# Kernel tuning notes

Measured on AMD Instinct MI355X. Metric: run time of the kernel, lower is better.

Reference implementation:

```python
import math
import jax, jax.numpy as jnp
import numpy as np

NUM_HEADS = 16
BASE = 10000.0


def _rope_sin_cos(seq_len, head_dim):
    # theta_j = pos / base^(2j/dim), j in [0, dim//2)
    j = jnp.arange(head_dim // 2, dtype=jnp.float32)
    inv_freq = jnp.power(jnp.float32(BASE), -2.0 * j / head_dim)  # [d/2]
    pos = jnp.arange(seq_len, dtype=jnp.float32)
    ang = pos[:, None] * inv_freq[None, :]          # [S, d/2]
    sin, cos = jnp.sin(ang), jnp.cos(ang)
    # interleave-repeat each entry twice: [S, d]
    sin2 = jnp.stack([sin, sin], axis=-1).reshape(seq_len, head_dim)
    cos2 = jnp.stack([cos, cos], axis=-1).reshape(seq_len, head_dim)
    return sin2, cos2


def _apply_rope(x, sin2, cos2):
    # x: [B, H, S, d]; rotate-half interleaved: (-x1, x0, -x3, x2, ...)
    x_even, x_odd = x[..., 0::2], x[..., 1::2]
    rot = jnp.stack([-x_odd, x_even], axis=-1).reshape(x.shape)
    return x * cos2 + rot * sin2


def setup_inputs() -> dict:
    key = jax.random.key(0)
    ks = jax.random.split(key, 9)
    B, S, H = 2, 2048, 2048
    sc = 1.0 / math.sqrt(H)
    return {
        "hidden_state": jax.random.normal(ks[0], (B, S, H), jnp.float32),
        "Wq": jax.random.normal(ks[1], (H, H), jnp.float32) * sc,
        "bq": jax.random.normal(ks[2], (H,), jnp.float32) * 0.01,
        "Wk": jax.random.normal(ks[3], (H, H), jnp.float32) * sc,
        "bk": jax.random.normal(ks[4], (H,), jnp.float32) * 0.01,
        "Wv": jax.random.normal(ks[5], (H, H), jnp.float32) * sc,
        "bv": jax.random.normal(ks[6], (H,), jnp.float32) * 0.01,
        "Wo": jax.random.normal(ks[7], (H, H), jnp.float32) * sc,
        "bo": jax.random.normal(ks[8], (H,), jnp.float32) * 0.01,
    }


def reference(hidden_state, Wq, bq, Wk, bk, Wv, bv, Wo, bo):
    B, S, H = hidden_state.shape
    nh = NUM_HEADS
    hd = H // nh

    def proj(W, b):
        y = jnp.einsum('bsh,hd->bsd', hidden_state, W) + b
        return y.reshape(B, S, nh, hd).transpose(0, 2, 1, 3)  # [B,nh,S,hd]

    q = proj(Wq, bq)
    k = proj(Wk, bk)
    v = proj(Wv, bv)

    sin2, cos2 = _rope_sin_cos(S, hd)  # [S, hd]
    q = _apply_rope(q, sin2, cos2)
    k = _apply_rope(k, sin2, cos2)

    scale = 1.0 / math.sqrt(hd)
    attn = jnp.einsum('bhqd,bhkd->bhqk', q, k) * scale  # [B,nh,S,S]
    attn = jax.nn.softmax(attn, axis=-1)
    out = jnp.einsum('bhqk,bhkd->bhqd', attn, v)
    out = out.transpose(0, 2, 1, 3).reshape(B, S, H)
    return jnp.einsum('bsh,hd->bsd', out, Wo) + bo
```

## Files before the change

### kernel.cpp

```cpp
#include <hip/hip_runtime.h>
#include <math.h>


typedef __bf16 bf16;
typedef __attribute__((ext_vector_type(8))) __bf16 bf16x8;
typedef __attribute__((ext_vector_type(4))) __bf16 bf16x4;
typedef __attribute__((ext_vector_type(4))) float f32x4;

#define S_LEN 2048
#define NHEAD 16
#define HD 128

__device__ __forceinline__ f32x4 mfma16(bf16x8 a, bf16x8 b, f32x4 c) {
    return __builtin_amdgcn_mfma_f32_16x16x32_bf16(a, b, c, 0, 0, 0);
}

__global__ __launch_bounds__(256) void cvt_f32_bf16(const float* __restrict__ x,
                                                    bf16* __restrict__ y, int n) {
    int i = (blockIdx.x * 256 + threadIdx.x) * 4;
    if (i + 3 < n) {
        const float4 v = *(const float4*)(x + i);
        bf16x4 o;
        o[0] = (bf16)v.x; o[1] = (bf16)v.y; o[2] = (bf16)v.z; o[3] = (bf16)v.w;
        *(bf16x4*)(y + i) = o;
    }
}

__global__ __launch_bounds__(128) void rope_tables(float* __restrict__ st,
                                                   float* __restrict__ ct) {
    const int s = blockIdx.x, d = threadIdx.x;
    const float invf = exp2f(-0.20762050593046013f * (float)(d >> 1));
    float sn, cs;
    sincosf((float)s * invf, &sn, &cs);
    st[(s << 7) | d] = sn;
    ct[(s << 7) | d] = cs;
}

__global__ __launch_bounds__(256) void transpose_cvt(const float* __restrict__ W,
                                                     bf16* __restrict__ Wt,
                                                     int Kd, int Nd) {
    __shared__ float tile[32][33];
    const int tx = threadIdx.x & 31, ty = threadIdx.x >> 5;
    const int bn = blockIdx.x * 32, bk = blockIdx.y * 32;
#pragma unroll
    for (int r = 0; r < 32; r += 8)
        tile[ty + r][tx] = W[(size_t)(bk + ty + r) * Nd + bn + tx];
    __syncthreads();
#pragma unroll
    for (int r = 0; r < 32; r += 8)
        Wt[(size_t)(bn + ty + r) * Kd + bk + tx] = (bf16)tile[tx][ty + r];
}

__global__ __launch_bounds__(256, 3)
void gemm_qkv(const bf16* __restrict__ A, const bf16* __restrict__ Bt,
              const float* __restrict__ bq, const float* __restrict__ bk,
              const float* __restrict__ bv, bf16* __restrict__ Qo,
              bf16* __restrict__ Ko, bf16* __restrict__ Vo,
              const float* __restrict__ stab, const float* __restrict__ ctab) {
    const int K = 2048;
    __shared__ __align__(16) bf16 smem[17408];
    bf16* As = smem;
    bf16* Bs = smem + 8192;
    const int t = threadIdx.x;
    const int w = t >> 6, l = t & 63;
    const int lr = l & 15, lq = l >> 4;
    const int m0 = blockIdx.y * 128, n0 = blockIdx.x * 128;
    const int wm = (w >> 1) * 64, wn = (w & 1) * 64;
    const int seg = n0 >> 11;
    const float* bias = (seg == 0) ? bq : (seg == 1) ? bk : bv;
    bf16* outB = (seg == 0) ? Qo : (seg == 1) ? Ko : Vo;

    f32x4 acc[4][4];
    const f32x4 fz = {0.f, 0.f, 0.f, 0.f};
#pragma unroll
    for (int i = 0; i < 4; ++i)
#pragma unroll
        for (int j = 0; j < 4; ++j) acc[i][j] = fz;

    bf16x8 rA[4], rB[4];
#pragma unroll
    for (int c = 0; c < 4; ++c) {
        const int chunk = c * 256 + t;
        const int row = chunk >> 3, cc = chunk & 7;
        rA[c] = *(const bf16x8*)&A[(size_t)(m0 + row) * K + cc * 8];
        rB[c] = *(const bf16x8*)&Bt[(size_t)(n0 + row) * K + cc * 8];
    }

    for (int k0 = 0; k0 < K; k0 += 64) {
#pragma unroll
        for (int c = 0; c < 4; ++c) {
            const int chunk = c * 256 + t;
            const int row = chunk >> 3, cc = chunk & 7;
            const int d = (row * 8 + (cc ^ (row & 7))) * 8;
            *(bf16x8*)&As[d] = rA[c];
            *(bf16x8*)&Bs[d] = rB[c];
        }
        __syncthreads();
        if (k0 + 64 < K) {
#pragma unroll
            for (int c = 0; c < 4; ++c) {
                const int chunk = c * 256 + t;
                const int row = chunk >> 3, cc = chunk & 7;
                rA[c] = *(const bf16x8*)&A[(size_t)(m0 + row) * K + k0 + 64 + cc * 8];
                rB[c] = *(const bf16x8*)&Bt[(size_t)(n0 + row) * K + k0 + 64 + cc * 8];
            }
        }
#pragma unroll
        for (int s = 0; s < 2; ++s) {
            bf16x8 af[4], bfr[4];
#pragma unroll
            for (int i = 0; i < 4; ++i) {
                const int row = wm + i * 16 + lr;
                af[i] = *(const bf16x8*)&As[(row * 8 + ((s * 4 + lq) ^ (row & 7))) * 8];
            }
#pragma unroll
            for (int j = 0; j < 4; ++j) {
                const int row = wn + j * 16 + lr;
                bfr[j] = *(const bf16x8*)&Bs[(row * 8 + ((s * 4 + lq) ^ (row & 7))) * 8];
            }
#pragma unroll
            for (int i = 0; i < 4; ++i)
#pragma unroll
                for (int j = 0; j < 4; ++j)
                    acc[i][j] = mfma16(af[i], bfr[j], acc[i][j]);
        }
        __syncthreads();
    }

    if (seg == 2) {
#pragma unroll
        for (int i = 0; i < 4; ++i) {
            const int rl0 = wm + i * 16 + lq * 4;
#pragma unroll
            for (int j = 0; j < 4; ++j) {
                const int cl = wn + j * 16 + lr;
                const float bv_ = bias[(n0 & 2047) + cl];
#pragma unroll
                for (int r = 0; r < 4; ++r)
                    smem[cl * 136 + rl0 + r] = (bf16)(acc[i][j][r] + bv_);
            }
        }
        __syncthreads();
        const int b = m0 >> 11;
#pragma unroll
        for (int p = 0; p < 8; ++p) {
            const int idx = p * 256 + t;
            const int col = idx >> 4, ch = idx & 15;
            const bf16x8 v = *(const bf16x8*)&smem[col * 136 + ch * 8];
            const int cg2 = (n0 & 2047) + col;
            const int h = cg2 >> 7, d = cg2 & 127;
            *(bf16x8*)&outB[((size_t)((b << 4) | h) * HD + d) * S_LEN +
                            (m0 & 2047) + ch * 8] = v;
        }
    } else {
#pragma unroll
        for (int i = 0; i < 4; ++i) {
            const int rg0 = m0 + wm + i * 16 + lq * 4;
#pragma unroll
            for (int j = 0; j < 4; ++j) {
                const int cg2 = (n0 & 2047) + wn + j * 16 + lr;
                const float bv_ = bias[cg2];
                const int h = cg2 >> 7, d = cg2 & 127;
#pragma unroll
                for (int r = 0; r < 4; ++r) {
                    const int rg = rg0 + r;
                    const int b = rg >> 11, s = rg & 2047;
                    float v = acc[i][j][r] + bv_;
                    float p = __shfl_xor(v, 1);
                    const float sn = stab[(s << 7) | d];
                    const float cs = ctab[(s << 7) | d];
                    float o = (d & 1) ? (v * cs + p * sn) : (v * cs - p * sn);
                    if (seg == 0) o *= 0.08838834764831843f;
                    outB[((size_t)((b << 4) + h) * S_LEN + s) * HD + d] = (bf16)o;
                }
            }
        }
    }
}

__global__ __launch_bounds__(256, 3)
void gemm_out(const bf16* __restrict__ A, const bf16* __restrict__ Bt,
              const float* __restrict__ bias, float* __restrict__ outF,
              int M, int N, int K) {
    __shared__ __align__(16) bf16 As[128 * 64];
    __shared__ __align__(16) bf16 Bs[128 * 64];
    const int t = threadIdx.x;
    const int w = t >> 6, l = t & 63;
    const int lr = l & 15, lq = l >> 4;
    const int m0 = blockIdx.y * 128, n0 = blockIdx.x * 128;
    const int wm = (w >> 1) * 64, wn = (w & 1) * 64;

    f32x4 acc[4][4];
    const f32x4 fz = {0.f, 0.f, 0.f, 0.f};
#pragma unroll
    for (int i = 0; i < 4; ++i)
#pragma unroll
        for (int j = 0; j < 4; ++j) acc[i][j] = fz;

    bf16x8 rA[4], rB[4];
#pragma unroll
    for (int c = 0; c < 4; ++c) {
        const int chunk = c * 256 + t;
        const int row = chunk >> 3, cc = chunk & 7;
        rA[c] = *(const bf16x8*)&A[(size_t)(m0 + row) * K + cc * 8];
        rB[c] = *(const bf16x8*)&Bt[(size_t)(n0 + row) * K + cc * 8];
    }

    for (int k0 = 0; k0 < K; k0 += 64) {
#pragma unroll
        for (int c = 0; c < 4; ++c) {
            const int chunk = c * 256 + t;
            const int row = chunk >> 3, cc = chunk & 7;
            const int d = (row * 8 + (cc ^ (row & 7))) * 8;
            *(bf16x8*)&As[d] = rA[c];
            *(bf16x8*)&Bs[d] = rB[c];
        }
        __syncthreads();
        if (k0 + 64 < K) {
#pragma unroll
            for (int c = 0; c < 4; ++c) {
                const int chunk = c * 256 + t;
                const int row = chunk >> 3, cc = chunk & 7;
                rA[c] = *(const bf16x8*)&A[(size_t)(m0 + row) * K + k0 + 64 + cc * 8];
                rB[c] = *(const bf16x8*)&Bt[(size_t)(n0 + row) * K + k0 + 64 + cc * 8];
            }
        }
#pragma unroll
        for (int s = 0; s < 2; ++s) {
            bf16x8 af[4], bfr[4];
#pragma unroll
            for (int i = 0; i < 4; ++i) {
                const int row = wm + i * 16 + lr;
                af[i] = *(const bf16x8*)&As[(row * 8 + ((s * 4 + lq) ^ (row & 7))) * 8];
            }
#pragma unroll
            for (int j = 0; j < 4; ++j) {
                const int row = wn + j * 16 + lr;
                bfr[j] = *(const bf16x8*)&Bs[(row * 8 + ((s * 4 + lq) ^ (row & 7))) * 8];
            }
#pragma unroll
            for (int i = 0; i < 4; ++i)
#pragma unroll
                for (int j = 0; j < 4; ++j)
                    acc[i][j] = mfma16(af[i], bfr[j], acc[i][j]);
        }
        __syncthreads();
    }
#pragma unroll
    for (int i = 0; i < 4; ++i) {
        const int rg0 = m0 + wm + i * 16 + lq * 4;
#pragma unroll
        for (int j = 0; j < 4; ++j) {
            const int cg = n0 + wn + j * 16 + lr;
            const float bv = bias[cg];
#pragma unroll
            for (int r = 0; r < 4; ++r)
                outF[(size_t)(rg0 + r) * N + cg] = acc[i][j][r] + bv;
        }
    }
}

__global__ __launch_bounds__(256, 2)
void attn_fwd(const bf16* __restrict__ Q, const bf16* __restrict__ K,
              const bf16* __restrict__ Vt, bf16* __restrict__ AO) {
    __shared__ __align__(16) bf16 Ks[64 * 128];
    __shared__ __align__(16) bf16 Vs[128 * 64];
    const int t = threadIdx.x;
    const int w = t >> 6, l = t & 63;
    const int lr = l & 15, lq = l >> 4;
    const int blk = blockIdx.x;
    const int qt = (blk >> 3) & 15;
    const int bh = ((blk & 7) << 2) | (blk >> 7);
    const int b = bh >> 4, h = bh & 15;

    const bf16* Qp = Q + (size_t)bh * S_LEN * HD;
    const bf16* Kp = K + (size_t)bh * S_LEN * HD;
    const bf16* Vp = Vt + (size_t)bh * HD * S_LEN;

    bf16x8 qf[2][4];
#pragma unroll
    for (int i = 0; i < 2; ++i)
#pragma unroll
        for (int s = 0; s < 4; ++s)
            qf[i][s] = *(const bf16x8*)&Qp[(size_t)(qt * 128 + w * 32 + i * 16 + lr) * HD +
                                           s * 32 + lq * 8];

    f32x4 O[2][8];
    const f32x4 fz = {0.f, 0.f, 0.f, 0.f};
#pragma unroll
    for (int i = 0; i < 2; ++i)
#pragma unroll
        for (int jd = 0; jd < 8; ++jd) O[i][jd] = fz;
    float lst[2][4] = {{0.f, 0.f, 0.f, 0.f}, {0.f, 0.f, 0.f, 0.f}};

    bf16x8 rK[4], rV[4];
#pragma unroll
    for (int c = 0; c < 4; ++c) {
        const int chunk = c * 256 + t;
        const int kr = chunk >> 4, kc = chunk & 15;
        const int vr = chunk >> 3, vc = chunk & 7;
        rK[c] = *(const bf16x8*)&Kp[(size_t)kr * HD + kc * 8];
        rV[c] = *(const bf16x8*)&Vp[(size_t)vr * S_LEN + vc * 8];
    }

    for (int kt = 0; kt < 32; ++kt) {
#pragma unroll
        for (int c = 0; c < 4; ++c) {
            const int chunk = c * 256 + t;
            const int kr = chunk >> 4, kc = chunk & 15;
            const int vr = chunk >> 3, vc = chunk & 7;
            *(bf16x8*)&Ks[(kr * 16 + (kc ^ (kr & 15))) * 8] = rK[c];
            *(bf16x8*)&Vs[(vr * 8 + (vc ^ (vr & 7))) * 8] = rV[c];
        }
        __syncthreads();

        if (kt < 31) {
#pragma unroll
            for (int c = 0; c < 4; ++c) {
                const int chunk = c * 256 + t;
                const int kr = chunk >> 4, kc = chunk & 15;
                const int vr = chunk >> 3, vc = chunk & 7;
                rK[c] = *(const bf16x8*)&Kp[(size_t)((kt + 1) * 64 + kr) * HD + kc * 8];
                rV[c] = *(const bf16x8*)&Vp[(size_t)vr * S_LEN + (kt + 1) * 64 + vc * 8];
            }
        }

        f32x4 Sc[2][4];
#pragma unroll
        for (int i = 0; i < 2; ++i)
#pragma unroll
            for (int j = 0; j < 4; ++j) Sc[i][j] = fz;
#pragma unroll
        for (int s = 0; s < 4; ++s) {
            bf16x8 kf[4];
#pragma unroll
            for (int j = 0; j < 4; ++j) {
                const int krow = j * 16 + lr;
                kf[j] = *(const bf16x8*)&Ks[(krow * 16 + ((s * 4 + lq) ^ (krow & 15))) * 8];
            }
#pragma unroll
            for (int i = 0; i < 2; ++i)
#pragma unroll
                for (int j = 0; j < 4; ++j)
                    Sc[i][j] = mfma16(qf[i][s], kf[j], Sc[i][j]);
        }
        __syncthreads();

        bf16* Ps = Ks;
#pragma unroll
        for (int i = 0; i < 2; ++i)
#pragma unroll
            for (int j = 0; j < 4; ++j)
#pragma unroll
                for (int r = 0; r < 4; ++r) {
                    const float p = __expf(Sc[i][j][r]);
                    lst[i][r] += p;
                    const int prow = w * 32 + i * 16 + lq * 4 + r;
                    const int pch = (j * 2 + (lr >> 3)) ^ (prow & 7);
                    Ps[(prow * 8 + pch) * 8 + (lr & 7)] = (bf16)p;
                }

#pragma unroll
        for (int s = 0; s < 2; ++s) {
            bf16x8 pf[2], vf[8];
#pragma unroll
            for (int i = 0; i < 2; ++i) {
                const int prow = w * 32 + i * 16 + lr;
                pf[i] = *(const bf16x8*)&Ps[(prow * 8 + ((s * 4 + lq) ^ (prow & 7))) * 8];
            }
#pragma unroll
            for (int jd = 0; jd < 8; ++jd) {
                const int vrow = jd * 16 + lr;
                vf[jd] = *(const bf16x8*)&Vs[(vrow * 8 + ((s * 4 + lq) ^ (vrow & 7))) * 8];
            }
#pragma unroll
            for (int i = 0; i < 2; ++i)
#pragma unroll
                for (int jd = 0; jd < 8; ++jd)
                    O[i][jd] = mfma16(pf[i], vf[jd], O[i][jd]);
        }
        __syncthreads();
    }

#pragma unroll
    for (int mask = 1; mask < 16; mask <<= 1)
#pragma unroll
        for (int i = 0; i < 2; ++i)
#pragma unroll
            for (int r = 0; r < 4; ++r) lst[i][r] += __shfl_xor(lst[i][r], mask);

#pragma unroll
    for (int i = 0; i < 2; ++i)
#pragma unroll
        for (int jd = 0; jd < 8; ++jd)
#pragma unroll
            for (int r = 0; r < 4; ++r) {
                const int srow = qt * 128 + w * 32 + i * 16 + lq * 4 + r;
                const float v = O[i][jd][r] / lst[i][r];
                AO[(size_t)(b * S_LEN + srow) * 2048 + h * HD + jd * 16 + lr] = (bf16)v;
            }
}

extern "C" void kernel_launch(void* const* d_in, const int* in_sizes, int n_in,
                              void* d_out, int out_size, void* d_ws, size_t ws_size,
                              hipStream_t stream) {
    const float* hs = (const float*)d_in[0];
    const float* Wq = (const float*)d_in[1];
    const float* bq = (const float*)d_in[2];
    const float* Wk = (const float*)d_in[3];
    const float* bk = (const float*)d_in[4];
    const float* Wv = (const float*)d_in[5];
    const float* bv = (const float*)d_in[6];
    const float* Wo = (const float*)d_in[7];
    const float* bo = (const float*)d_in[8];
    float* out = (float*)d_out;

    char* ws = (char*)d_ws;
    bf16* Xb = (bf16*)ws;
    bf16* Wt3 = (bf16*)(ws + (size_t)16777216);
    bf16* Qb = (bf16*)(ws + (size_t)41943040);
    bf16* Kb = (bf16*)(ws + (size_t)58720256);
    bf16* Vb = (bf16*)(ws + (size_t)75497472);
    float* stab = (float*)(ws + (size_t)92274688);
    float* ctab = (float*)(ws + (size_t)93323264);
    bf16* AO = Xb;

    const dim3 tg(64, 64);

    rope_tables<<<2048, 128, 0, stream>>>(stab, ctab);
    cvt_f32_bf16<<<8192, 256, 0, stream>>>(hs, Xb, 8388608);
    transpose_cvt<<<tg, 256, 0, stream>>>(Wq, Wt3, 2048, 2048);
    transpose_cvt<<<tg, 256, 0, stream>>>(Wk, Wt3 + (size_t)2048 * 2048, 2048, 2048);
    transpose_cvt<<<tg, 256, 0, stream>>>(Wv, Wt3 + (size_t)2 * 2048 * 2048, 2048, 2048);
    gemm_qkv<<<dim3(48, 32), 256, 0, stream>>>(Xb, Wt3, bq, bk, bv, Qb, Kb, Vb,
                                               stab, ctab);
    attn_fwd<<<512, 256, 0, stream>>>(Qb, Kb, Vb, AO);
    transpose_cvt<<<tg, 256, 0, stream>>>(Wo, Wt3, 2048, 2048);
    gemm_out<<<dim3(16, 32), 256, 0, stream>>>(AO, Wt3, bo, out, 4096, 2048, 2048);
}
```

Baseline: 406.1 us.

## Rewrite QKV GEMM with 256x256 tiles and async global-to-LDS double buffering

The QKV projection GEMM now uses 512-thread blocks computing 256x256 output tiles. Operands are loaded straight into a double-buffered LDS ring with global_load_lds, and the loads are interleaved with four MFMA phases per k-step under barriers, sched_barrier and setprio. The goal is to overlap global loads with MFMA work, skip the register staging copy, and raise data reuse per tile. The V-path epilogue now transposes per warp through LDS. The cost is 128KB of LDS and high register pressure, which limits occupancy to one or two blocks per CU, and the grid shrinks to 384 blocks, which may leave some CUs unevenly loaded.

```diff
diff --git a/kernel.cpp b/kernel.cpp
--- a/kernel.cpp
+++ b/kernel.cpp
@@ -14,6 +14,21 @@
 __device__ __forceinline__ f32x4 mfma16(bf16x8 a, bf16x8 b, f32x4 c) {
     return __builtin_amdgcn_mfma_f32_16x16x32_bf16(a, b, c, 0, 0, 0);
 }
+
+__device__ __forceinline__ void gload16(const bf16* g, bf16* s) {
+    __builtin_amdgcn_global_load_lds(
+        (const __attribute__((address_space(1))) void*)g,
+        (__attribute__((address_space(3))) void*)s, 16, 0, 0);
+}
+
+#define BAR()                                  \
+    do {                                       \
+        asm volatile("" ::: "memory");         \
+        __builtin_amdgcn_s_barrier();          \
+        asm volatile("" ::: "memory");         \
+    } while (0)
+#define WAITV(n) asm volatile("s_waitcnt vmcnt(" #n ")" ::: "memory")
+#define SCHED0() __builtin_amdgcn_sched_barrier(0)
 
 __global__ __launch_bounds__(256) void cvt_f32_bf16(const float* __restrict__ x,
                                                     bf16* __restrict__ y, int n) {
@@ -51,121 +66,202 @@
         Wt[(size_t)(bn + ty + r) * Kd + bk + tx] = (bf16)tile[tx][ty + r];
 }
 
-__global__ __launch_bounds__(256, 3)
+#define STG_A(kt, reg)                                                        \
+    do {                                                                      \
+        bf16* d_ = smem + (((((kt) & 1) << 1) + (reg)) << 13);                \
+        const size_t ko_ = (size_t)((kt) << 6) + ((size_t)(reg) << 17);       \
+        gload16(A + aoff0 + ko_, d_ + loff0);                                 \
+        gload16(A + aoff1 + ko_, d_ + loff1);                                 \
+    } while (0)
+#define STG_B(kt, reg)                                                        \
+    do {                                                                      \
+        bf16* d_ = smem + 32768 + (((((kt) & 1) << 1) + (reg)) << 13);        \
+        const size_t ko_ = (size_t)((kt) << 6) + ((size_t)(reg) << 16);       \
+        gload16(Bt + boff0 + ko_, d_ + loff0);                                \
+        gload16(Bt + boff1 + ko_, d_ + loff1);                                \
+    } while (0)
+
+__global__ __launch_bounds__(512, 2)
 void gemm_qkv(const bf16* __restrict__ A, const bf16* __restrict__ Bt,
               const float* __restrict__ bq, const float* __restrict__ bk,
               const float* __restrict__ bv, bf16* __restrict__ Qo,
               bf16* __restrict__ Ko, bf16* __restrict__ Vo,
               const float* __restrict__ stab, const float* __restrict__ ctab) {
-    const int K = 2048;
-    __shared__ __align__(16) bf16 smem[17408];
-    bf16* As = smem;
-    bf16* Bs = smem + 8192;
-    const int t = threadIdx.x;
-    const int w = t >> 6, l = t & 63;
+    __shared__ __align__(16) bf16 smem[65536];
+    const int tid = threadIdx.x;
+    const int w = tid >> 6, l = tid & 63;
     const int lr = l & 15, lq = l >> 4;
-    const int m0 = blockIdx.y * 128, n0 = blockIdx.x * 128;
-    const int wm = (w >> 1) * 64, wn = (w & 1) * 64;
+    const int wr = w >> 2, wc = w & 3;
+    const int m0 = blockIdx.y * 256, n0 = blockIdx.x * 256;
+
+    size_t aoff0, aoff1, boff0, boff1;
+    {
+        const int ch0 = tid, ch1 = 512 + tid;
+        const int rl0 = ch0 >> 3, rl1 = ch1 >> 3;
+        const int cc0 = (ch0 & 7) ^ (rl0 & 7), cc1 = (ch1 & 7) ^ (rl1 & 7);
+        aoff0 = (size_t)(m0 + (rl0 & 63) + ((rl0 >> 6) << 7)) * 2048 + (cc0 << 3);
+        aoff1 = (size_t)(m0 + (rl1 & 63) + ((rl1 >> 6) << 7)) * 2048 + (cc1 << 3);
+        boff0 = (size_t)(n0 + (rl0 & 31) + ((rl0 >> 5) << 6)) * 2048 + (cc0 << 3);
+        boff1 = (size_t)(n0 + (rl1 & 31) + ((rl1 >> 5) << 6)) * 2048 + (cc1 << 3);
+    }
+    const int loff0 = tid << 3, loff1 = 4096 + (tid << 3);
+
+    f32x4 acc[8][4];
+    const f32x4 fz = {0.f, 0.f, 0.f, 0.f};
+#pragma unroll
+    for (int i = 0; i < 8; ++i)
+#pragma unroll
+        for (int j = 0; j < 4; ++j) acc[i][j] = fz;
+
+    STG_A(0, 0); STG_B(0, 0); STG_B(0, 1); STG_A(0, 1);
+    STG_A(1, 0); STG_B(1, 0); STG_A(1, 1);
+    WAITV(6);
+    BAR();
+
+    const int csel0 = ((0 * 4 + lq) ^ (lr & 7)) << 3;
+    const int csel1 = ((1 * 4 + lq) ^ (lr & 7)) << 3;
+    const int arow = (wr * 64 + lr) << 6;
+    const int brow = (wc * 32 + lr) << 6;
+
+#pragma unroll 2
+    for (int t = 0; t < 32; ++t) {
+        const int buf = t & 1;
+        const int abase = (buf << 1) << 13;
+        const int bbase = 32768 + ((buf << 1) << 13);
+        bf16x8 a[4][2], b0[2][2], b1[2][2];
+
+#pragma unroll
+        for (int i = 0; i < 4; ++i) {
+            a[i][0] = *(const bf16x8*)&smem[abase + arow + (i << 10) + csel0];
+            a[i][1] = *(const bf16x8*)&smem[abase + arow + (i << 10) + csel1];
+        }
+#pragma unroll
+        for (int j = 0; j < 2; ++j) {
+            b0[j][0] = *(const bf16x8*)&smem[bbase + brow + (j << 10) + csel0];
+            b0[j][1] = *(const bf16x8*)&smem[bbase + brow + (j << 10) + csel1];
+        }
+        if (t + 1 < 32) STG_B(t + 1, 1);
+        BAR();
+        SCHED0();
+        __builtin_amdgcn_s_setprio(1);
+#pragma unroll
+        for (int i = 0; i < 4; ++i)
+#pragma unroll
+            for (int j = 0; j < 2; ++j) {
+                acc[i][j] = mfma16(a[i][0], b0[j][0], acc[i][j]);
+                acc[i][j] = mfma16(a[i][1], b0[j][1], acc[i][j]);
+            }
+        __builtin_amdgcn_s_setprio(0);
+        SCHED0();
+        BAR();
+
+#pragma unroll
+        for (int j = 0; j < 2; ++j) {
+            b1[j][0] = *(const bf16x8*)&smem[bbase + 8192 + brow + (j << 10) + csel0];
+            b1[j][1] = *(const bf16x8*)&smem[bbase + 8192 + brow + (j << 10) + csel1];
+        }
+        if (t + 2 < 32) STG_A(t + 2, 0);
+        BAR();
+        SCHED0();
+        __builtin_amdgcn_s_setprio(1);
+#pragma unroll
+        for (int i = 0; i < 4; ++i)
+#pragma unroll
+            for (int j = 0; j < 2; ++j) {
+                acc[i][2 + j] = mfma16(a[i][0], b1[j][0], acc[i][2 + j]);
+                acc[i][2 + j] = mfma16(a[i][1], b1[j][1], acc[i][2 + j]);
+            }
+        __builtin_amdgcn_s_setprio(0);
+        SCHED0();
+        BAR();
+
+#pragma unroll
+        for (int i = 0; i < 4; ++i) {
+            a[i][0] = *(const bf16x8*)&smem[abase + 8192 + arow + (i << 10) + csel0];
+            a[i][1] = *(const bf16x8*)&smem[abase + 8192 + arow + (i << 10) + csel1];
+        }
+        if (t + 2 < 32) STG_B(t + 2, 0);
+        BAR();
+        SCHED0();
+        __builtin_amdgcn_s_setprio(1);
+#pragma unroll
+        for (int i = 0; i < 4; ++i)
+#pragma unroll
+            for (int j = 0; j < 2; ++j) {
+                acc[4 + i][2 + j] = mfma16(a[i][0], b1[j][0], acc[4 + i][2 + j]);
+                acc[4 + i][2 + j] = mfma16(a[i][1], b1[j][1], acc[4 + i][2 + j]);
+            }
+        __builtin_amdgcn_s_setprio(0);
+        SCHED0();
+        BAR();
+
+        if (t + 2 < 32) STG_A(t + 2, 1);
+        BAR();
+        SCHED0();
+        __builtin_amdgcn_s_setprio(1);
+#pragma unroll
+        for (int i = 0; i < 4; ++i)
+#pragma unroll
+            for (int j = 0; j < 2; ++j) {
+                acc[4 + i][j] = mfma16(a[i][0], b0[j][0], acc[4 + i][j]);
+                acc[4 + i][j] = mfma16(a[i][1], b0[j][1], acc[4 + i][j]);
+            }
+        __builtin_amdgcn_s_setprio(0);
+        SCHED0();
+        if (t + 2 < 32) {
+            WAITV(6);
+        } else if (t + 1 < 32) {
+            WAITV(0);
+        }
+        BAR();
+    }
+
     const int seg = n0 >> 11;
     const float* bias = (seg == 0) ? bq : (seg == 1) ? bk : bv;
-    bf16* outB = (seg == 0) ? Qo : (seg == 1) ? Ko : Vo;
-
-    f32x4 acc[4][4];
-    const f32x4 fz = {0.f, 0.f, 0.f, 0.f};
-#pragma unroll
-    for (int i = 0; i < 4; ++i)
-#pragma unroll
-        for (int j = 0; j < 4; ++j) acc[i][j] = fz;
-
-    bf16x8 rA[4], rB[4];
-#pragma unroll
-    for (int c = 0; c < 4; ++c) {
-        const int chunk = c * 256 + t;
-        const int row = chunk >> 3, cc = chunk & 7;
-        rA[c] = *(const bf16x8*)&A[(size_t)(m0 + row) * K + cc * 8];
-        rB[c] = *(const bf16x8*)&Bt[(size_t)(n0 + row) * K + cc * 8];
-    }
-
-    for (int k0 = 0; k0 < K; k0 += 64) {
-#pragma unroll
-        for (int c = 0; c < 4; ++c) {
-            const int chunk = c * 256 + t;
-            const int row = chunk >> 3, cc = chunk & 7;
-            const int d = (row * 8 + (cc ^ (row & 7))) * 8;
-            *(bf16x8*)&As[d] = rA[c];
-            *(bf16x8*)&Bs[d] = rB[c];
-        }
-        __syncthreads();
-        if (k0 + 64 < K) {
-#pragma unroll
-            for (int c = 0; c < 4; ++c) {
-                const int chunk = c * 256 + t;
-                const int row = chunk >> 3, cc = chunk & 7;
-                rA[c] = *(const bf16x8*)&A[(size_t)(m0 + row) * K + k0 + 64 + cc * 8];
-                rB[c] = *(const bf16x8*)&Bt[(size_t)(n0 + row) * K + k0 + 64 + cc * 8];
-            }
-        }
-#pragma unroll
-        for (int s = 0; s < 2; ++s) {
-            bf16x8 af[4], bfr[4];
-#pragma unroll
-            for (int i = 0; i < 4; ++i) {
-                const int row = wm + i * 16 + lr;
-                af[i] = *(const bf16x8*)&As[(row * 8 + ((s * 4 + lq) ^ (row & 7))) * 8];
-            }
-#pragma unroll
-            for (int j = 0; j < 4; ++j) {
-                const int row = wn + j * 16 + lr;
-                bfr[j] = *(const bf16x8*)&Bs[(row * 8 + ((s * 4 + lq) ^ (row & 7))) * 8];
-            }
-#pragma unroll
-            for (int i = 0; i < 4; ++i)
-#pragma unroll
-                for (int j = 0; j < 4; ++j)
-                    acc[i][j] = mfma16(af[i], bfr[j], acc[i][j]);
-        }
-        __syncthreads();
-    }
-
     if (seg == 2) {
-#pragma unroll
-        for (int i = 0; i < 4; ++i) {
-            const int rl0 = wm + i * 16 + lq * 4;
-#pragma unroll
-            for (int j = 0; j < 4; ++j) {
-                const int cl = wn + j * 16 + lr;
-                const float bv_ = bias[(n0 & 2047) + cl];
-#pragma unroll
-                for (int r = 0; r < 4; ++r)
-                    smem[cl * 136 + rl0 + r] = (bf16)(acc[i][j][r] + bv_);
-            }
-        }
-        __syncthreads();
+        bf16* lt = smem + w * 4608;
+        const int cgb = (n0 & 2047) + wc * 64;
+        const int h = cgb >> 7, d0 = cgb & 127;
         const int b = m0 >> 11;
-#pragma unroll
-        for (int p = 0; p < 8; ++p) {
-            const int idx = p * 256 + t;
-            const int col = idx >> 4, ch = idx & 15;
-            const bf16x8 v = *(const bf16x8*)&smem[col * 136 + ch * 8];
-            const int cg2 = (n0 & 2047) + col;
-            const int h = cg2 >> 7, d = cg2 & 127;
-            *(bf16x8*)&outB[((size_t)((b << 4) | h) * HD + d) * S_LEN +
-                            (m0 & 2047) + ch * 8] = v;
+        const int sb = (m0 & 2047) + wr * 128;
+#pragma unroll
+        for (int mh = 0; mh < 2; ++mh) {
+#pragma unroll
+            for (int mi = 0; mi < 4; ++mi)
+#pragma unroll
+                for (int nj = 0; nj < 4; ++nj) {
+                    const int cl = ((nj >> 1) << 5) + ((nj & 1) << 4) + lr;
+                    const float bv_ = bias[cgb + cl];
+#pragma unroll
+                    for (int r = 0; r < 4; ++r)
+                        lt[cl * 72 + mi * 16 + lq * 4 + r] =
+                            (bf16)(acc[mh * 4 + mi][nj][r] + bv_);
+                }
+#pragma unroll
+            for (int p = 0; p < 8; ++p) {
+                const int dl = p * 8 + (l >> 3);
+                const int sc = l & 7;
+                const bf16x8 v = *(const bf16x8*)&lt[dl * 72 + sc * 8];
+                *(bf16x8*)&Vo[((size_t)((b << 4) | h) * HD + d0 + dl) * S_LEN +
+                              sb + mh * 64 + sc * 8] = v;
+            }
         }
     } else {
-#pragma unroll
-        for (int i = 0; i < 4; ++i) {
-            const int rg0 = m0 + wm + i * 16 + lq * 4;
-#pragma unroll
-            for (int j = 0; j < 4; ++j) {
-                const int cg2 = (n0 & 2047) + wn + j * 16 + lr;
+        bf16* outB = (seg == 0) ? Qo : Ko;
+#pragma unroll
+        for (int mi = 0; mi < 8; ++mi) {
+            const int rg0 = m0 + wr * 128 + ((mi >> 2) << 6) + ((mi & 3) << 4) + (lq << 2);
+#pragma unroll
+            for (int nj = 0; nj < 4; ++nj) {
+                const int cg2 = (n0 & 2047) + wc * 64 + ((nj >> 1) << 5) +
+                                ((nj & 1) << 4) + lr;
                 const float bv_ = bias[cg2];
                 const int h = cg2 >> 7, d = cg2 & 127;
 #pragma unroll
                 for (int r = 0; r < 4; ++r) {
                     const int rg = rg0 + r;
                     const int b = rg >> 11, s = rg & 2047;
-                    float v = acc[i][j][r] + bv_;
+                    float v = acc[mi][nj][r] + bv_;
                     float p = __shfl_xor(v, 1);
                     const float sn = stab[(s << 7) | d];
                     const float cs = ctab[(s << 7) | d];
@@ -432,7 +528,7 @@
     transpose_cvt<<<tg, 256, 0, stream>>>(Wq, Wt3, 2048, 2048);
     transpose_cvt<<<tg, 256, 0, stream>>>(Wk, Wt3 + (size_t)2048 * 2048, 2048, 2048);
     transpose_cvt<<<tg, 256, 0, stream>>>(Wv, Wt3 + (size_t)2 * 2048 * 2048, 2048, 2048);
-    gemm_qkv<<<dim3(48, 32), 256, 0, stream>>>(Xb, Wt3, bq, bk, bv, Qb, Kb, Vb,
+    gemm_qkv<<<dim3(24, 16), 512, 0, stream>>>(Xb, Wt3, bq, bk, bv, Qb, Kb, Vb,
                                                stab, ctab);
     attn_fwd<<<512, 256, 0, stream>>>(Qb, Kb, Vb, AO);
     transpose_cvt<<<tg, 256, 0, stream>>>(Wo, Wt3, 2048, 2048);
```

After: 403.0 us. About the same (-0.8%).
